# Kernel tuning notes

Measured on AMD Instinct MI355X. Metric: run time of the kernel, lower is better.

Reference implementation:

```python
import jax, jax.numpy as jnp
import numpy as np
import math

B, S, E, H = 4, 2048, 1024, 16
HD = E // H

def setup_inputs() -> dict:
    key = jax.random.key(0)
    ks = jax.random.split(key, 5)
    lim_qkv = math.sqrt(6.0 / (E + 3 * E))  # xavier_uniform for (3E, E)
    lim_out = math.sqrt(6.0 / (E + E))
    return {
        "x": jax.random.normal(ks[0], (B, S, E), dtype=jnp.float32),
        "qkv_w": jax.random.uniform(ks[1], (3 * E, E), minval=-lim_qkv, maxval=lim_qkv, dtype=jnp.float32),
        "qkv_b": jnp.zeros((3 * E,), dtype=jnp.float32),
        "out_w": jax.random.uniform(ks[2], (E, E), minval=-lim_out, maxval=lim_out, dtype=jnp.float32),
        "out_b": jnp.zeros((E,), dtype=jnp.float32),
    }

def reference(x, qkv_w, qkv_b, out_w, out_b):
    bsz, seq_len, embed_dim = x.shape
    scale = math.sqrt(HD)
    # fused QKV projection (torch Linear: x @ W.T + b)
    qkv = x @ qkv_w.T + qkv_b                      # [B, S, 3E]
    # per-head layout: slice [h*3hd:(h+1)*3hd] holds (q,k,v) for head h
    qkv = qkv.reshape(bsz, seq_len, H, 3, HD)       # [B, S, H, 3, hd]
    q = jnp.transpose(qkv[:, :, :, 0, :], (0, 2, 1, 3))  # [B, H, S, hd]
    k = jnp.transpose(qkv[:, :, :, 1, :], (0, 2, 1, 3))
    v = jnp.transpose(qkv[:, :, :, 2, :], (0, 2, 1, 3))
    scores = jnp.einsum("bhqd,bhkd->bhqk", q, k) / scale
    causal = jnp.tril(jnp.ones((seq_len, seq_len), dtype=bool))
    scores = jnp.where(causal[None, None], scores, -jnp.inf)
    attn = jax.nn.softmax(scores, axis=-1)          # dropout = identity (eval mode)
    out = jnp.einsum("bhqk,bhkd->bhqd", attn, v)    # [B, H, S, hd]
    out = jnp.transpose(out, (0, 2, 1, 3)).reshape(bsz, seq_len, embed_dim)
    return out @ out_w.T + out_b
```

## Files before the change

### kernel.cpp

```cpp
#include <hip/hip_runtime.h>
#include <hip/hip_bf16.h>
#include <cstdint>

#define NB 4
#define NS 2048
#define NE 1024
#define NH 16

typedef __attribute__((ext_vector_type(8))) short bf16x8;
typedef __attribute__((ext_vector_type(4))) float f32x4;

__device__ __forceinline__ unsigned short f2bf(float f) {
  unsigned u = __float_as_uint(f);
  u += 0x7fffu + ((u >> 16) & 1u);
  return (unsigned short)(u >> 16);
}

__device__ __forceinline__ unsigned pk2bf(float lo, float hi) {
  return __builtin_amdgcn_perm(__float_as_uint(hi) + 0x8000u,
                               __float_as_uint(lo) + 0x8000u, 0x07060302u);
}

__device__ __forceinline__ float exp2_fast(float x) {
#if __has_builtin(__builtin_amdgcn_exp2f)
  return __builtin_amdgcn_exp2f(x);
#else
  float r;
  asm("v_exp_f32 %0, %1" : "=v"(r) : "v"(x));
  return r;
#endif
}

__device__ __forceinline__ void gl_lds16(const void* g, void* l) {
  __builtin_amdgcn_global_load_lds(
      (const __attribute__((address_space(1))) void*)g,
      (__attribute__((address_space(3))) void*)l, 16, 0, 0);
}

__global__ __launch_bounds__(256) void cast_k(const float* __restrict__ in,
                                              unsigned short* __restrict__ out, int n4) {
  int idx = blockIdx.x * 256 + threadIdx.x;
  if (idx >= n4) return;
  float4 v = ((const float4*)in)[idx];
  ushort4 o;
  o.x = f2bf(v.x); o.y = f2bf(v.y); o.z = f2bf(v.z); o.w = f2bf(v.w);
  ((ushort4*)out)[idx] = o;
}

template <int MODE>
__global__ __launch_bounds__(256, 2) void gemm_bt(
    const unsigned short* __restrict__ A,
    const unsigned short* __restrict__ Bm,
    const float* __restrict__ bias,
    void* __restrict__ Cv,
    unsigned short* __restrict__ Qp,
    unsigned short* __restrict__ Kp,
    unsigned short* __restrict__ Vp,
    int M, int N, int K) {
  __shared__ __align__(16) unsigned short As[128 * 64];
  __shared__ __align__(16) unsigned short Bs[128 * 64];
  const int tid = threadIdx.x;
  const int lane = tid & 63, wave = tid >> 6;
  const int m0 = blockIdx.y * 128, n0 = blockIdx.x * 128;
  const int wm = (wave >> 1) * 64, wn = (wave & 1) * 64;
  const int fr = lane & 15, fq = lane >> 4;

  f32x4 acc[4][4];
#pragma unroll
  for (int i = 0; i < 4; i++)
#pragma unroll
    for (int j = 0; j < 4; j++) acc[i][j] = (f32x4){0.f, 0.f, 0.f, 0.f};

  const int srow = lane >> 3;
  const int scol = ((lane & 7) ^ srow) * 8;

  for (int kt = 0; kt < K; kt += 64) {
    __syncthreads();
#pragma unroll
    for (int c = 0; c < 4; c++) {
      const int chunk = wave * 4 + c;
      const int row = chunk * 8 + srow;
      gl_lds16(A + (size_t)(m0 + row) * K + kt + scol, As + chunk * 512);
      gl_lds16(Bm + (size_t)(n0 + row) * K + kt + scol, Bs + chunk * 512);
    }
    __syncthreads();
#pragma unroll
    for (int s = 0; s < 2; s++) {
      bf16x8 af[4], bf[4];
#pragma unroll
      for (int i = 0; i < 4; i++)
        af[i] = *(const bf16x8*)(As + (wm + i * 16 + fr) * 64 +
                                 (((s * 4 + fq) ^ (fr & 7)) * 8));
#pragma unroll
      for (int j = 0; j < 4; j++)
        bf[j] = *(const bf16x8*)(Bs + (wn + j * 16 + fr) * 64 +
                                 (((s * 4 + fq) ^ (fr & 7)) * 8));
#pragma unroll
      for (int i = 0; i < 4; i++)
#pragma unroll
        for (int j = 0; j < 4; j++)
          acc[i][j] = __builtin_amdgcn_mfma_f32_16x16x32_bf16(af[i], bf[j], acc[i][j], 0, 0, 0);
    }
  }

#pragma unroll
  for (int j = 0; j < 4; j++) {
    const int col = n0 + wn + j * 16 + fr;
    const float bval = bias[col];
    const int h = col / 192, rr = col - h * 192;
#pragma unroll
    for (int i = 0; i < 4; i++)
#pragma unroll
      for (int r = 0; r < 4; r++) {
        const int row = m0 + wm + i * 16 + fq * 4 + r;
        float v = acc[i][j][r] + bval;
        if (MODE == 0) {
          ((float*)Cv)[(size_t)row * N + col] = v;
        } else {
          const int b = row >> 11, s = row & 2047;
          const int bh = b * 16 + h;
          if (rr < 64) {
            Qp[((size_t)bh * 2048 + s) * 64 + rr] = f2bf(v * 0.1803368802f);
          } else if (rr < 128) {
            Kp[((size_t)bh * 2048 + s) * 64 + (rr - 64)] = f2bf(v);
          } else {
            Vp[((size_t)bh * 64 + (rr - 128)) * 2048 + s] = f2bf(v);
          }
        }
      }
  }
}

#define LDP 72
__global__ __launch_bounds__(128, 2) void attn_k(
    const unsigned short* __restrict__ Qg, const unsigned short* __restrict__ Kg,
    const unsigned short* __restrict__ Vg, unsigned short* __restrict__ outa) {
  __shared__ __align__(16) unsigned short Ks[64 * 64];
  __shared__ __align__(16) unsigned short VTs[64 * 64];
  __shared__ __align__(16) unsigned short Ps[2 * 32 * LDP];
  const int tid = threadIdx.x;
  const int lane = tid & 63, wave = tid >> 6;
  const int fc = lane & 15, fq = lane >> 4, fc7 = fc & 7;
  const int bh = blockIdx.y;
  const int b = bh >> 4, h = bh & 15;
  const int srow = lane >> 3;
  const int scol = ((lane & 7) ^ srow) * 8;
  const unsigned short* Qb = Qg + (size_t)bh * 2048 * 64;
  const unsigned short* Kb = Kg + (size_t)bh * 2048 * 64;
  const unsigned short* Vb = Vg + (size_t)bh * 64 * 2048;
  unsigned short* Pw = Ps + wave * 32 * LDP;

#pragma unroll 1
  for (int phase = 0; phase < 2; phase++) {
    const int qt = phase ? 31 - (int)blockIdx.x : (int)blockIdx.x;
    const int qw = qt * 64 + wave * 32;

    bf16x8 qb[2][2];
#pragma unroll
    for (int g = 0; g < 2; g++) {
      const unsigned short* qrow = Qb + (size_t)(qw + g * 16 + fc) * 64;
      qb[g][0] = *(const bf16x8*)(qrow + fq * 8);
      qb[g][1] = *(const bf16x8*)(qrow + 32 + fq * 8);
    }

    f32x4 O[4][2];
#pragma unroll
    for (int dt = 0; dt < 4; dt++)
#pragma unroll
      for (int g = 0; g < 2; g++) O[dt][g] = (f32x4){0.f, 0.f, 0.f, 0.f};
    float msx[2] = {-3e38f, -3e38f}, lsx[2] = {0.f, 0.f};

#pragma unroll 1
    for (int kb = 0; kb <= qt; kb++) {
      const int k0 = kb * 64;
      __syncthreads();
#pragma unroll
      for (int c = 0; c < 4; c++) {
        const int rbase = c * 16 + wave * 8;
        gl_lds16(Kb + (size_t)(k0 + rbase + srow) * 64 + scol, Ks + rbase * 64);
        gl_lds16(Vb + (size_t)(rbase + srow) * 2048 + k0 + scol, VTs + rbase * 64);
      }
      __syncthreads();

      f32x4 S[4][2];
#pragma unroll
      for (int t = 0; t < 4; t++) {
        bf16x8 ka0 = *(const bf16x8*)(Ks + (t * 16 + fc) * 64 + ((fq ^ fc7) * 8));
        bf16x8 ka1 = *(const bf16x8*)(Ks + (t * 16 + fc) * 64 + (((4 + fq) ^ fc7) * 8));
#pragma unroll
        for (int g = 0; g < 2; g++) {
          f32x4 s = (f32x4){0.f, 0.f, 0.f, 0.f};
          s = __builtin_amdgcn_mfma_f32_16x16x32_bf16(ka0, qb[g][0], s, 0, 0, 0);
          s = __builtin_amdgcn_mfma_f32_16x16x32_bf16(ka1, qb[g][1], s, 0, 0, 0);
          S[t][g] = s;
        }
      }
      if (kb == qt) {
#pragma unroll
        for (int t = 0; t < 4; t++)
#pragma unroll
          for (int g = 0; g < 2; g++)
#pragma unroll
            for (int r = 0; r < 4; r++)
              if (k0 + t * 16 + fq * 4 + r > qw + g * 16 + fc) S[t][g][r] = -3e38f;
      }
      float alpha[2];
#pragma unroll
      for (int g = 0; g < 2; g++) {
        float cm = S[0][g][0];
#pragma unroll
        for (int t = 0; t < 4; t++)
#pragma unroll
          for (int r = 0; r < 4; r++) cm = fmaxf(cm, S[t][g][r]);
        cm = fmaxf(cm, __shfl_xor(cm, 16, 64));
        cm = fmaxf(cm, __shfl_xor(cm, 32, 64));
        float mn = fmaxf(msx[g], cm);
        alpha[g] = exp2_fast(msx[g] - mn);
        msx[g] = mn;
        float ps = 0.f;
#pragma unroll
        for (int t = 0; t < 4; t++)
#pragma unroll
          for (int r = 0; r < 4; r++) {
            float p = exp2_fast(S[t][g][r] - mn);
            S[t][g][r] = p;
            ps += p;
          }
        ps += __shfl_xor(ps, 16, 64);
        ps += __shfl_xor(ps, 32, 64);
        lsx[g] = lsx[g] * alpha[g] + ps;
      }
#pragma unroll
      for (int g = 0; g < 2; g++)
#pragma unroll
        for (int t = 0; t < 4; t++) {
          uint2 u;
          u.x = pk2bf(S[t][g][0], S[t][g][1]);
          u.y = pk2bf(S[t][g][2], S[t][g][3]);
          *(uint2*)(Pw + (g * 16 + fc) * LDP + t * 16 + fq * 4) = u;
        }
      bf16x8 pb[2][2];
#pragma unroll
      for (int g = 0; g < 2; g++)
#pragma unroll
        for (int s = 0; s < 2; s++)
          pb[g][s] = *(const bf16x8*)(Pw + (g * 16 + fc) * LDP + s * 32 + fq * 8);
#pragma unroll
      for (int dt = 0; dt < 4; dt++)
#pragma unroll
        for (int g = 0; g < 2; g++)
#pragma unroll
          for (int r = 0; r < 4; r++) O[dt][g][r] *= alpha[g];
#pragma unroll
      for (int dt = 0; dt < 4; dt++) {
        bf16x8 va0 = *(const bf16x8*)(VTs + (dt * 16 + fc) * 64 + ((fq ^ fc7) * 8));
        bf16x8 va1 = *(const bf16x8*)(VTs + (dt * 16 + fc) * 64 + (((4 + fq) ^ fc7) * 8));
#pragma unroll
        for (int g = 0; g < 2; g++) {
          O[dt][g] = __builtin_amdgcn_mfma_f32_16x16x32_bf16(va0, pb[g][0], O[dt][g], 0, 0, 0);
          O[dt][g] = __builtin_amdgcn_mfma_f32_16x16x32_bf16(va1, pb[g][1], O[dt][g], 0, 0, 0);
        }
      }
    }

    float inv[2] = {1.f / lsx[0], 1.f / lsx[1]};
#pragma unroll
    for (int dt = 0; dt < 4; dt++)
#pragma unroll
      for (int g = 0; g < 2; g++) {
        uint2 u;
        u.x = pk2bf(O[dt][g][0] * inv[g], O[dt][g][1] * inv[g]);
        u.y = pk2bf(O[dt][g][2] * inv[g], O[dt][g][3] * inv[g]);
        size_t row = (size_t)(b * NS) + qw + g * 16 + fc;
        *(uint2*)(outa + row * 1024 + h * 64 + dt * 16 + fq * 4) = u;
      }
    __syncthreads();
  }
}

extern "C" void kernel_launch(void* const* d_in, const int* in_sizes, int n_in,
                              void* d_out, int out_size, void* d_ws, size_t ws_size,
                              hipStream_t stream) {
  const float* x     = (const float*)d_in[0];
  const float* qkv_w = (const float*)d_in[1];
  const float* qkv_b = (const float*)d_in[2];
  const float* out_w = (const float*)d_in[3];
  const float* out_b = (const float*)d_in[4];

  unsigned short* xb   = (unsigned short*)d_ws;
  unsigned short* wqkv = xb + (size_t)8192 * 1024;
  unsigned short* wo   = wqkv + (size_t)3072 * 1024;
  unsigned short* Qg   = wo + (size_t)1024 * 1024;
  unsigned short* Kg   = Qg + (size_t)64 * 2048 * 64;
  unsigned short* Vg   = Kg + (size_t)64 * 2048 * 64;
  unsigned short* att  = Vg + (size_t)64 * 64 * 2048;

  cast_k<<<(2097152 + 255) / 256, 256, 0, stream>>>(x, xb, 2097152);
  cast_k<<<(786432 + 255) / 256, 256, 0, stream>>>(qkv_w, wqkv, 786432);
  cast_k<<<(262144 + 255) / 256, 256, 0, stream>>>(out_w, wo, 262144);

  gemm_bt<1><<<dim3(24, 64), 256, 0, stream>>>(xb, wqkv, qkv_b, nullptr,
                                               Qg, Kg, Vg, 8192, 3072, 1024);
  attn_k<<<dim3(16, 64), 128, 0, stream>>>(Qg, Kg, Vg, att);
  gemm_bt<0><<<dim3(8, 64), 256, 0, stream>>>(att, wo, out_b, d_out,
                                              nullptr, nullptr, nullptr,
                                              8192, 1024, 1024);
}
```

Before: 284.9 us.

## Double-buffer K/V tiles, lazy softmax rescale, swizzle P tile, XCD-aware grid

```diff
diff --git a/kernel.cpp b/kernel.cpp
--- a/kernel.cpp
+++ b/kernel.cpp
@@ -131,28 +131,29 @@
   }
 }
 
-#define LDP 72
 __global__ __launch_bounds__(128, 2) void attn_k(
     const unsigned short* __restrict__ Qg, const unsigned short* __restrict__ Kg,
     const unsigned short* __restrict__ Vg, unsigned short* __restrict__ outa) {
-  __shared__ __align__(16) unsigned short Ks[64 * 64];
-  __shared__ __align__(16) unsigned short VTs[64 * 64];
-  __shared__ __align__(16) unsigned short Ps[2 * 32 * LDP];
+  __shared__ __align__(16) unsigned short Ks[2 * 64 * 64];
+  __shared__ __align__(16) unsigned short VTs[2 * 64 * 64];
+  __shared__ __align__(16) unsigned short Ps[2 * 32 * 64];
   const int tid = threadIdx.x;
   const int lane = tid & 63, wave = tid >> 6;
   const int fc = lane & 15, fq = lane >> 4, fc7 = fc & 7;
-  const int bh = blockIdx.y;
+  const int wg = ((int)blockIdx.x & 7) * 128 + ((int)blockIdx.x >> 3);
+  const int bh = wg >> 4, qx = wg & 15;
   const int b = bh >> 4, h = bh & 15;
   const int srow = lane >> 3;
   const int scol = ((lane & 7) ^ srow) * 8;
+  const int pswz = fc & 14;
   const unsigned short* Qb = Qg + (size_t)bh * 2048 * 64;
   const unsigned short* Kb = Kg + (size_t)bh * 2048 * 64;
   const unsigned short* Vb = Vg + (size_t)bh * 64 * 2048;
-  unsigned short* Pw = Ps + wave * 32 * LDP;
+  unsigned short* Pw = Ps + wave * 32 * 64;
 
 #pragma unroll 1
   for (int phase = 0; phase < 2; phase++) {
-    const int qt = phase ? 31 - (int)blockIdx.x : (int)blockIdx.x;
+    const int qt = phase ? 31 - qx : qx;
     const int qw = qt * 64 + wave * 32;
 
     bf16x8 qb[2][2];
@@ -170,23 +171,38 @@
       for (int g = 0; g < 2; g++) O[dt][g] = (f32x4){0.f, 0.f, 0.f, 0.f};
     float msx[2] = {-3e38f, -3e38f}, lsx[2] = {0.f, 0.f};
 
+#pragma unroll
+    for (int c = 0; c < 4; c++) {
+      const int rbase = c * 16 + wave * 8;
+      gl_lds16(Kb + (size_t)(rbase + srow) * 64 + scol, Ks + rbase * 64);
+      gl_lds16(Vb + (size_t)(rbase + srow) * 2048 + scol, VTs + rbase * 64);
+    }
+    __syncthreads();
+
 #pragma unroll 1
     for (int kb = 0; kb <= qt; kb++) {
+      const int bsel = kb & 1;
+      if (kb < qt) {
+        const int k0n = (kb + 1) * 64;
+        unsigned short* Kd = Ks + (bsel ^ 1) * 4096;
+        unsigned short* Vd = VTs + (bsel ^ 1) * 4096;
+#pragma unroll
+        for (int c = 0; c < 4; c++) {
+          const int rbase = c * 16 + wave * 8;
+          gl_lds16(Kb + (size_t)(k0n + rbase + srow) * 64 + scol, Kd + rbase * 64);
+          gl_lds16(Vb + (size_t)(rbase + srow) * 2048 + k0n + scol, Vd + rbase * 64);
+        }
+      }
       const int k0 = kb * 64;
-      __syncthreads();
-#pragma unroll
-      for (int c = 0; c < 4; c++) {
-        const int rbase = c * 16 + wave * 8;
-        gl_lds16(Kb + (size_t)(k0 + rbase + srow) * 64 + scol, Ks + rbase * 64);
-        gl_lds16(Vb + (size_t)(rbase + srow) * 2048 + k0 + scol, VTs + rbase * 64);
-      }
-      __syncthreads();
+      const unsigned short* Ksb = Ks + bsel * 4096;
+      const unsigned short* VTb = VTs + bsel * 4096;
 
       f32x4 S[4][2];
+      __builtin_amdgcn_s_setprio(1);
 #pragma unroll
       for (int t = 0; t < 4; t++) {
-        bf16x8 ka0 = *(const bf16x8*)(Ks + (t * 16 + fc) * 64 + ((fq ^ fc7) * 8));
-        bf16x8 ka1 = *(const bf16x8*)(Ks + (t * 16 + fc) * 64 + (((4 + fq) ^ fc7) * 8));
+        bf16x8 ka0 = *(const bf16x8*)(Ksb + (t * 16 + fc) * 64 + ((fq ^ fc7) * 8));
+        bf16x8 ka1 = *(const bf16x8*)(Ksb + (t * 16 + fc) * 64 + (((4 + fq) ^ fc7) * 8));
 #pragma unroll
         for (int g = 0; g < 2; g++) {
           f32x4 s = (f32x4){0.f, 0.f, 0.f, 0.f};
@@ -195,6 +211,7 @@
           S[t][g] = s;
         }
       }
+      __builtin_amdgcn_s_setprio(0);
       if (kb == qt) {
 #pragma unroll
         for (int t = 0; t < 4; t++)
@@ -205,30 +222,32 @@
               if (k0 + t * 16 + fq * 4 + r > qw + g * 16 + fc) S[t][g][r] = -3e38f;
       }
       float alpha[2];
+      bool resc = false;
 #pragma unroll
       for (int g = 0; g < 2; g++) {
-        float cm = S[0][g][0];
-#pragma unroll
-        for (int t = 0; t < 4; t++)
-#pragma unroll
-          for (int r = 0; r < 4; r++) cm = fmaxf(cm, S[t][g][r]);
+        float c0 = fmaxf(fmaxf(S[0][g][0], S[0][g][1]), fmaxf(S[0][g][2], S[0][g][3]));
+        float c1 = fmaxf(fmaxf(S[1][g][0], S[1][g][1]), fmaxf(S[1][g][2], S[1][g][3]));
+        float c2 = fmaxf(fmaxf(S[2][g][0], S[2][g][1]), fmaxf(S[2][g][2], S[2][g][3]));
+        float c3 = fmaxf(fmaxf(S[3][g][0], S[3][g][1]), fmaxf(S[3][g][2], S[3][g][3]));
+        float cm = fmaxf(fmaxf(c0, c1), fmaxf(c2, c3));
         cm = fmaxf(cm, __shfl_xor(cm, 16, 64));
         cm = fmaxf(cm, __shfl_xor(cm, 32, 64));
-        float mn = fmaxf(msx[g], cm);
-        alpha[g] = exp2_fast(msx[g] - mn);
-        msx[g] = mn;
-        float ps = 0.f;
-#pragma unroll
-        for (int t = 0; t < 4; t++)
-#pragma unroll
-          for (int r = 0; r < 4; r++) {
-            float p = exp2_fast(S[t][g][r] - mn);
-            S[t][g][r] = p;
-            ps += p;
-          }
-        ps += __shfl_xor(ps, 16, 64);
-        ps += __shfl_xor(ps, 32, 64);
-        lsx[g] = lsx[g] * alpha[g] + ps;
+        if (__all(cm - msx[g] <= 8.0f)) {
+          alpha[g] = 1.0f;
+        } else {
+          const float mn = fmaxf(msx[g], cm);
+          alpha[g] = exp2_fast(msx[g] - mn);
+          msx[g] = mn;
+          resc = true;
+        }
+        float ps[4];
+#pragma unroll
+        for (int t = 0; t < 4; t++) {
+#pragma unroll
+          for (int r = 0; r < 4; r++) S[t][g][r] = exp2_fast(S[t][g][r] - msx[g]);
+          ps[t] = (S[t][g][0] + S[t][g][1]) + (S[t][g][2] + S[t][g][3]);
+        }
+        lsx[g] = fmaf(lsx[g], alpha[g], (ps[0] + ps[1]) + (ps[2] + ps[3]));
       }
 #pragma unroll
       for (int g = 0; g < 2; g++)
@@ -237,33 +256,46 @@
           uint2 u;
           u.x = pk2bf(S[t][g][0], S[t][g][1]);
           u.y = pk2bf(S[t][g][2], S[t][g][3]);
-          *(uint2*)(Pw + (g * 16 + fc) * LDP + t * 16 + fq * 4) = u;
+          *(uint2*)(Pw + (g * 16 + fc) * 64 + (((t * 4 + fq) ^ pswz) * 4)) = u;
         }
       bf16x8 pb[2][2];
 #pragma unroll
       for (int g = 0; g < 2; g++)
 #pragma unroll
         for (int s = 0; s < 2; s++)
-          pb[g][s] = *(const bf16x8*)(Pw + (g * 16 + fc) * LDP + s * 32 + fq * 8);
-#pragma unroll
-      for (int dt = 0; dt < 4; dt++)
-#pragma unroll
-        for (int g = 0; g < 2; g++)
-#pragma unroll
-          for (int r = 0; r < 4; r++) O[dt][g][r] *= alpha[g];
+          pb[g][s] = *(const bf16x8*)(Pw + (g * 16 + fc) * 64 +
+                                      (((s * 8 + fq * 2) ^ pswz) * 4));
+      if (resc) {
+#pragma unroll
+        for (int dt = 0; dt < 4; dt++)
+#pragma unroll
+          for (int g = 0; g < 2; g++)
+#pragma unroll
+            for (int r = 0; r < 4; r++) O[dt][g][r] *= alpha[g];
+      }
+      __builtin_amdgcn_s_setprio(1);
 #pragma unroll
       for (int dt = 0; dt < 4; dt++) {
-        bf16x8 va0 = *(const bf16x8*)(VTs + (dt * 16 + fc) * 64 + ((fq ^ fc7) * 8));
-        bf16x8 va1 = *(const bf16x8*)(VTs + (dt * 16 + fc) * 64 + (((4 + fq) ^ fc7) * 8));
+        bf16x8 va0 = *(const bf16x8*)(VTb + (dt * 16 + fc) * 64 + ((fq ^ fc7) * 8));
+        bf16x8 va1 = *(const bf16x8*)(VTb + (dt * 16 + fc) * 64 + (((4 + fq) ^ fc7) * 8));
 #pragma unroll
         for (int g = 0; g < 2; g++) {
           O[dt][g] = __builtin_amdgcn_mfma_f32_16x16x32_bf16(va0, pb[g][0], O[dt][g], 0, 0, 0);
           O[dt][g] = __builtin_amdgcn_mfma_f32_16x16x32_bf16(va1, pb[g][1], O[dt][g], 0, 0, 0);
         }
       }
-    }
-
-    float inv[2] = {1.f / lsx[0], 1.f / lsx[1]};
+      __builtin_amdgcn_s_setprio(0);
+      __syncthreads();
+    }
+
+    float inv[2];
+#pragma unroll
+    for (int g = 0; g < 2; g++) {
+      float l = lsx[g];
+      l += __shfl_xor(l, 16, 64);
+      l += __shfl_xor(l, 32, 64);
+      inv[g] = 1.f / l;
+    }
 #pragma unroll
     for (int dt = 0; dt < 4; dt++)
 #pragma unroll
@@ -274,7 +306,6 @@
         size_t row = (size_t)(b * NS) + qw + g * 16 + fc;
         *(uint2*)(outa + row * 1024 + h * 64 + dt * 16 + fq * 4) = u;
       }
-    __syncthreads();
   }
 }
 
@@ -301,7 +332,7 @@
 
   gemm_bt<1><<<dim3(24, 64), 256, 0, stream>>>(xb, wqkv, qkv_b, nullptr,
                                                Qg, Kg, Vg, 8192, 3072, 1024);
-  attn_k<<<dim3(16, 64), 128, 0, stream>>>(Qg, Kg, Vg, att);
+  attn_k<<<dim3(1024), 128, 0, stream>>>(Qg, Kg, Vg, att);
   gemm_bt<0><<<dim3(8, 64), 256, 0, stream>>>(att, wo, out_b, d_out,
                                               nullptr, nullptr, nullptr,
                                               8192, 1024, 1024);
```

Result: faster. 256.2 us (-10.1%).
